# Optimization experiments

Hardware: AMD Instinct MI355X
Metric: run time of the kernel (lower is better)

## Reference

```python
import jax, jax.numpy as jnp
import numpy as np

NUM_HEADS = 8
EMBED_DIM = 64
HEAD_DIM = EMBED_DIM // NUM_HEADS
B, N, T = 2, 512, 24


def setup_inputs() -> dict:
    key = jax.random.key(0)
    ks = jax.random.split(key, 8)
    shp = (B, N, T, EMBED_DIM)
    return {
        "values": jax.random.normal(ks[0], shp, jnp.float32),
        "keys": jax.random.normal(ks[1], shp, jnp.float32),
        "query": jax.random.normal(ks[2], shp, jnp.float32),
        "Wv": jax.random.normal(ks[3], (HEAD_DIM, HEAD_DIM), jnp.float32) / np.sqrt(HEAD_DIM),
        "Wk": jax.random.normal(ks[4], (HEAD_DIM, HEAD_DIM), jnp.float32) / np.sqrt(HEAD_DIM),
        "Wq": jax.random.normal(ks[5], (HEAD_DIM, HEAD_DIM), jnp.float32) / np.sqrt(HEAD_DIM),
        "Wo": jax.random.normal(ks[6], (EMBED_DIM, EMBED_DIM), jnp.float32) / np.sqrt(EMBED_DIM),
        "bo": jnp.zeros((EMBED_DIM,), jnp.float32),
    }


def reference(values, keys, query, Wv, Wk, Wq, Wo, bo):
    b, n, t, e = query.shape
    h, d = NUM_HEADS, HEAD_DIM
    # split heads: (b, n, t, h, d)
    v = values.reshape(b, n, t, h, d) @ Wv.T
    k = keys.reshape(b, n, t, h, d) @ Wk.T
    q = query.reshape(b, n, t, h, d) @ Wq.T
    # node-axis attention per (timestep, head)
    energy = jnp.einsum('bqthd,bkthd->bqkth', q, k)  # (b, q_nodes, k_nodes, t, h)
    attn = jax.nn.softmax(energy / jnp.sqrt(jnp.float32(e)), axis=2)
    out = jnp.einsum('bqkth,bkthd->bqthd', attn, v).reshape(b, n, t, h * d)
    return out @ Wo.T + bo
```

## Files before the change

kernel.cpp:

```cpp
#include <hip/hip_runtime.h>

#define NUM_HEADS 8
#define EMBED 64
#define BB 2
#define NN 512
#define TT 24

typedef _Float16 half4v __attribute__((ext_vector_type(4)));
typedef _Float16 half2v __attribute__((ext_vector_type(2)));
typedef __fp16   fp16x2 __attribute__((ext_vector_type(2)));
typedef __fp16   fp16x4 __attribute__((ext_vector_type(4)));
typedef float    f32x4  __attribute__((ext_vector_type(4)));

#define KSTRIDE 20
#define VSTRIDE 524

__global__ __launch_bounds__(256) void attn_kernel(
    const float* __restrict__ values,
    const float* __restrict__ keys,
    const float* __restrict__ query,
    const float* __restrict__ Wv,
    const float* __restrict__ Wk,
    const float* __restrict__ Wq,
    float* __restrict__ out)
{
    __shared__ float w[192];
    __shared__ __align__(16) _Float16 Kpad[NN * KSTRIDE];
    __shared__ __align__(16) _Float16 Qpad[256 * KSTRIDE];
    __shared__ __align__(16) _Float16 Vt[16 * VSTRIDE];

    const int tid  = threadIdx.x;
    const int half = blockIdx.x >= 384;
    const int grp  = blockIdx.x - half * 384;
    const int h = grp & 7;
    const int t = (grp >> 3) % TT;
    const int b = grp / (8 * TT);

    const int r0 = 2 * tid;
    const long base0 = ((long)(b * NN + r0) * TT + t) * EMBED + h * 8;
    const long base1 = base0 + (long)TT * EMBED;
    const long qbase = ((long)(b * NN + half * 256 + tid) * TT + t) * EMBED + h * 8;
    float4 ka0 = *(const float4*)(keys + base0);
    float4 ka1 = *(const float4*)(keys + base0 + 4);
    float4 kb0 = *(const float4*)(keys + base1);
    float4 kb1 = *(const float4*)(keys + base1 + 4);
    float4 va0 = *(const float4*)(values + base0);
    float4 va1 = *(const float4*)(values + base0 + 4);
    float4 vb0 = *(const float4*)(values + base1);
    float4 vb1 = *(const float4*)(values + base1 + 4);
    float4 q0 = *(const float4*)(query + qbase);
    float4 q1 = *(const float4*)(query + qbase + 4);

    if (tid < 192) {
        float v;
        if (tid < 64)       v = Wq[tid];
        else if (tid < 128) v = Wk[tid - 64];
        else                v = Wv[tid - 128];
        w[tid] = v;
    }
    {
        unsigned int* z = (unsigned int*)(Vt + 8 * VSTRIDE);
        for (int i = tid; i < 8 * VSTRIDE / 2; i += 256)
            z[i] = (i < VSTRIDE / 2) ? 0x3C003C00u : 0u;
    }
    __syncthreads();

    {
        float k0[8] = {ka0.x, ka0.y, ka0.z, ka0.w, ka1.x, ka1.y, ka1.z, ka1.w};
        float k1[8] = {kb0.x, kb0.y, kb0.z, kb0.w, kb1.x, kb1.y, kb1.z, kb1.w};
        float v0[8] = {va0.x, va0.y, va0.z, va0.w, va1.x, va1.y, va1.z, va1.w};
        float v1[8] = {vb0.x, vb0.y, vb0.z, vb0.w, vb1.x, vb1.y, vb1.z, vb1.w};
        half4v klo0, khi0, klo1, khi1;
        #pragma unroll
        for (int dp = 0; dp < 8; ++dp) {
            float sk0 = 0.f, sk1 = 0.f, sv0 = 0.f, sv1 = 0.f;
            #pragma unroll
            for (int d = 0; d < 8; ++d) {
                const float wk = w[64 + dp * 8 + d], wvv = w[128 + dp * 8 + d];
                sk0 += k0[d] * wk;  sk1 += k1[d] * wk;
                sv0 += v0[d] * wvv; sv1 += v1[d] * wvv;
            }
            if (dp < 4) { klo0[dp] = (_Float16)sk0; klo1[dp] = (_Float16)sk1; }
            else        { khi0[dp - 4] = (_Float16)sk0; khi1[dp - 4] = (_Float16)sk1; }
            half2v vv = {(_Float16)sv0, (_Float16)sv1};
            *(half2v*)(Vt + dp * VSTRIDE + r0) = vv;
        }
        const half4v zz = {(_Float16)0.f, (_Float16)0.f, (_Float16)0.f, (_Float16)0.f};
        *(half4v*)(Kpad + r0 * KSTRIDE)            = klo0;
        *(half4v*)(Kpad + r0 * KSTRIDE + 4)        = khi0;
        *(half4v*)(Kpad + r0 * KSTRIDE + 8)        = zz;
        *(half4v*)(Kpad + r0 * KSTRIDE + 12)       = zz;
        *(half4v*)(Kpad + (r0 + 1) * KSTRIDE)      = klo1;
        *(half4v*)(Kpad + (r0 + 1) * KSTRIDE + 4)  = khi1;
        *(half4v*)(Kpad + (r0 + 1) * KSTRIDE + 8)  = zz;
        *(half4v*)(Kpad + (r0 + 1) * KSTRIDE + 12) = zz;

        float qx[8] = {q0.x, q0.y, q0.z, q0.w, q1.x, q1.y, q1.z, q1.w};
        const float scale = 0.125f * 1.44269504088896340736f;
        half4v qlo, qhi;
        #pragma unroll
        for (int dp = 0; dp < 8; ++dp) {
            float s = 0.f;
            #pragma unroll
            for (int d = 0; d < 8; ++d) s += qx[d] * w[dp * 8 + d];
            s *= scale;
            if (dp < 4) qlo[dp] = (_Float16)s; else qhi[dp - 4] = (_Float16)s;
        }
        *(half4v*)(Qpad + tid * KSTRIDE)      = qlo;
        *(half4v*)(Qpad + tid * KSTRIDE + 4)  = qhi;
        *(half4v*)(Qpad + tid * KSTRIDE + 8)  = zz;
        *(half4v*)(Qpad + tid * KSTRIDE + 12) = zz;
    }
    __syncthreads();

    const int wv   = tid >> 6;
    const int lane = tid & 63;
    const int ln   = lane & 15;
    const int quad = lane >> 4;
    const f32x4 zero4 = {0.f, 0.f, 0.f, 0.f};

    #pragma unroll 1
    for (int pass = 0; pass < 2; ++pass) {
        const int ql0 = pass * 128 + wv * 32;
        const half4v Qa = *(const half4v*)(Qpad + (ql0 + ln) * KSTRIDE + quad * 4);
        const half4v Qb = *(const half4v*)(Qpad + (ql0 + 16 + ln) * KSTRIDE + quad * 4);
        f32x4 Oa = {0.f, 0.f, 0.f, 0.f};
        f32x4 Ob = {0.f, 0.f, 0.f, 0.f};
        #pragma unroll 4
        for (int kt = 0; kt < 32; ++kt) {
            half4v Kf = *(const half4v*)(Kpad + (kt * 16 + ln) * KSTRIDE + quad * 4);
            half4v Vf = *(const half4v*)(Vt + ln * VSTRIDE + kt * 16 + quad * 4);
            f32x4 Ea = __builtin_amdgcn_mfma_f32_16x16x16f16(Kf, Qa, zero4, 0, 0, 0);
            f32x4 Eb = __builtin_amdgcn_mfma_f32_16x16x16f16(Kf, Qb, zero4, 0, 0, 0);
            fp16x2 pa0 = __builtin_amdgcn_cvt_pkrtz(__builtin_amdgcn_exp2f(Ea[0]),
                                                    __builtin_amdgcn_exp2f(Ea[1]));
            fp16x2 pa1 = __builtin_amdgcn_cvt_pkrtz(__builtin_amdgcn_exp2f(Ea[2]),
                                                    __builtin_amdgcn_exp2f(Ea[3]));
            fp16x2 pb0 = __builtin_amdgcn_cvt_pkrtz(__builtin_amdgcn_exp2f(Eb[0]),
                                                    __builtin_amdgcn_exp2f(Eb[1]));
            fp16x2 pb1 = __builtin_amdgcn_cvt_pkrtz(__builtin_amdgcn_exp2f(Eb[2]),
                                                    __builtin_amdgcn_exp2f(Eb[3]));
            half4v Pa = __builtin_bit_cast(half4v,
                (fp16x4)__builtin_shufflevector(pa0, pa1, 0, 1, 2, 3));
            half4v Pb = __builtin_bit_cast(half4v,
                (fp16x4)__builtin_shufflevector(pb0, pb1, 0, 1, 2, 3));
            Oa = __builtin_amdgcn_mfma_f32_16x16x16f16(Vf, Pa, Oa, 0, 0, 0);
            Ob = __builtin_amdgcn_mfma_f32_16x16x16f16(Vf, Pb, Ob, 0, 0, 0);
        }
        const float la = __shfl(Oa[0], 32 + ln, 64);
        const float lb = __shfl(Ob[0], 32 + ln, 64);
        const float ia = 1.0f / la;
        const float ib = 1.0f / lb;
        if (lane < 32) {
            const long oa = ((long)(b * NN + half * 256 + ql0 + ln) * TT + t) * EMBED
                          + h * 8 + quad * 4;
            const long ob = ((long)(b * NN + half * 256 + ql0 + 16 + ln) * TT + t) * EMBED
                          + h * 8 + quad * 4;
            *(float4*)(out + oa) = make_float4(Oa[0] * ia, Oa[1] * ia, Oa[2] * ia, Oa[3] * ia);
            *(float4*)(out + ob) = make_float4(Ob[0] * ib, Ob[1] * ib, Ob[2] * ib, Ob[3] * ib);
        }
    }
}

#define PSTRIDE 68
__global__ __launch_bounds__(256) void proj_kernel(
    const float* __restrict__ Wo,
    const float* __restrict__ bo,
    float* __restrict__ io)
{
    __shared__ float As[64 * PSTRIDE];
    __shared__ float WsT[64 * PSTRIDE];
    __shared__ float bos[EMBED];

    const int tid = threadIdx.x;
    const int row0 = blockIdx.x * 64;

    {
        const int r = tid >> 2;
        const int seg = tid & 3;
        #pragma unroll
        for (int i = 0; i < 4; ++i) {
            const int c = seg * 16 + i * 4;
            float4 av = *(const float4*)(io + (long)(row0 + r) * 64 + c);
            *(float4*)(As + r * PSTRIDE + c) = av;
        }
        #pragma unroll
        for (int i = 0; i < 16; ++i) {
            const int idx = tid + i * 256;
            WsT[(idx & 63) * PSTRIDE + (idx >> 6)] = Wo[idx];
        }
        if (tid < 64) bos[tid] = bo[tid];
    }
    __syncthreads();

    const int rg = tid >> 4;
    const int cg = tid & 15;
    float c[4][4] = {};
    #pragma unroll
    for (int kq = 0; kq < 16; ++kq) {
        float4 a[4], wt[4];
        #pragma unroll
        for (int i = 0; i < 4; ++i)
            a[i] = *(const float4*)(As + (rg * 4 + i) * PSTRIDE + kq * 4);
        #pragma unroll
        for (int kk = 0; kk < 4; ++kk)
            wt[kk] = *(const float4*)(WsT + (kq * 4 + kk) * PSTRIDE + cg * 4);
        #pragma unroll
        for (int i = 0; i < 4; ++i) {
            c[i][0] += a[i].x * wt[0].x + a[i].y * wt[1].x + a[i].z * wt[2].x + a[i].w * wt[3].x;
            c[i][1] += a[i].x * wt[0].y + a[i].y * wt[1].y + a[i].z * wt[2].y + a[i].w * wt[3].y;
            c[i][2] += a[i].x * wt[0].z + a[i].y * wt[1].z + a[i].z * wt[2].z + a[i].w * wt[3].z;
            c[i][3] += a[i].x * wt[0].w + a[i].y * wt[1].w + a[i].z * wt[2].w + a[i].w * wt[3].w;
        }
    }
    #pragma unroll
    for (int i = 0; i < 4; ++i) {
        float4 o = make_float4(c[i][0] + bos[cg * 4 + 0],
                               c[i][1] + bos[cg * 4 + 1],
                               c[i][2] + bos[cg * 4 + 2],
                               c[i][3] + bos[cg * 4 + 3]);
        *(float4*)(io + (long)(row0 + rg * 4 + i) * 64 + cg * 4) = o;
    }
}

extern "C" void kernel_launch(void* const* d_in, const int* in_sizes, int n_in,
                              void* d_out, int out_size, void* d_ws, size_t ws_size,
                              hipStream_t stream) {
    const float* values = (const float*)d_in[0];
    const float* keys   = (const float*)d_in[1];
    const float* query  = (const float*)d_in[2];
    const float* Wv     = (const float*)d_in[3];
    const float* Wk     = (const float*)d_in[4];
    const float* Wq     = (const float*)d_in[5];
    const float* Wo     = (const float*)d_in[6];
    const float* bo     = (const float*)d_in[7];
    float* out = (float*)d_out;

    (void)in_sizes; (void)n_in; (void)out_size; (void)d_ws; (void)ws_size;

    attn_kernel<<<BB * TT * NUM_HEADS * 2, 256, 0, stream>>>(
        values, keys, query, Wv, Wk, Wq, out);
    proj_kernel<<<(BB * NN * TT) / 64, 256, 0, stream>>>(Wo, bo, out);
}
```

Measured before the change: 116.4 us.

## Use fp16 MFMA for output projection and remap attention block indices

The output projection kernel is rewritten to drop its shared-memory fp32 FMA tiling. Each wavefront now loads 16 rows straight from global memory, converts them and Wo to fp16, and computes the result with 16x16x32 MFMA instructions, removing the LDS staging and the barrier. The attention kernel's block-to-(b,t,h,half) mapping is permuted so blocks are spread across XCDs differently, which may improve L2 locality for shared K/V data. The fp16 conversion lowers projection precision, and the output writes become scalar and strided.

```diff
diff --git a/kernel.cpp b/kernel.cpp
--- a/kernel.cpp
+++ b/kernel.cpp
@@ -8,6 +8,7 @@
 
 typedef _Float16 half4v __attribute__((ext_vector_type(4)));
 typedef _Float16 half2v __attribute__((ext_vector_type(2)));
+typedef _Float16 half8v __attribute__((ext_vector_type(8)));
 typedef __fp16   fp16x2 __attribute__((ext_vector_type(2)));
 typedef __fp16   fp16x4 __attribute__((ext_vector_type(4)));
 typedef float    f32x4  __attribute__((ext_vector_type(4)));
@@ -29,12 +30,15 @@
     __shared__ __align__(16) _Float16 Qpad[256 * KSTRIDE];
     __shared__ __align__(16) _Float16 Vt[16 * VSTRIDE];
 
-    const int tid  = threadIdx.x;
-    const int half = blockIdx.x >= 384;
-    const int grp  = blockIdx.x - half * 384;
-    const int h = grp & 7;
-    const int t = (grp >> 3) % TT;
-    const int b = grp / (8 * TT);
+    const int tid = threadIdx.x;
+    const int Bidx = blockIdx.x;
+    const int wi   = ((Bidx & 7) * 96) + (Bidx >> 3);
+    const int sub  = wi & 3;
+    const int rest = wi >> 2;
+    const int half = sub >> 1;
+    const int h    = ((rest & 3) << 1) | (sub & 1);
+    const int t    = (rest >> 2) % TT;
+    const int b    = rest / 96;
 
     const int r0 = 2 * tid;
     const long base0 = ((long)(b * NN + r0) * TT + t) * EMBED + h * 8;
@@ -162,64 +166,50 @@
     }
 }
 
-#define PSTRIDE 68
 __global__ __launch_bounds__(256) void proj_kernel(
     const float* __restrict__ Wo,
     const float* __restrict__ bo,
     float* __restrict__ io)
 {
-    __shared__ float As[64 * PSTRIDE];
-    __shared__ float WsT[64 * PSTRIDE];
-    __shared__ float bos[EMBED];
-
-    const int tid = threadIdx.x;
-    const int row0 = blockIdx.x * 64;
-
-    {
-        const int r = tid >> 2;
-        const int seg = tid & 3;
+    const int tid  = threadIdx.x;
+    const int wv   = tid >> 6;
+    const int lane = tid & 63;
+    const int ln   = lane & 15;
+    const int quad = lane >> 4;
+    const int row0 = blockIdx.x * 64 + wv * 16;
+
+    const float* arow = io + (long)(row0 + ln) * EMBED + quad * 8;
+    float4 a0 = *(const float4*)(arow);
+    float4 a1 = *(const float4*)(arow + 4);
+    float4 a2 = *(const float4*)(arow + 32);
+    float4 a3 = *(const float4*)(arow + 36);
+    half8v Af1, Af2;
+    Af1[0]=(_Float16)a0.x; Af1[1]=(_Float16)a0.y; Af1[2]=(_Float16)a0.z; Af1[3]=(_Float16)a0.w;
+    Af1[4]=(_Float16)a1.x; Af1[5]=(_Float16)a1.y; Af1[6]=(_Float16)a1.z; Af1[7]=(_Float16)a1.w;
+    Af2[0]=(_Float16)a2.x; Af2[1]=(_Float16)a2.y; Af2[2]=(_Float16)a2.z; Af2[3]=(_Float16)a2.w;
+    Af2[4]=(_Float16)a3.x; Af2[5]=(_Float16)a3.y; Af2[6]=(_Float16)a3.z; Af2[7]=(_Float16)a3.w;
+
+    #pragma unroll
+    for (int nt = 0; nt < 4; ++nt) {
+        const float* wrow = Wo + (long)(nt * 16 + ln) * EMBED + quad * 8;
+        float4 w0 = *(const float4*)(wrow);
+        float4 w1 = *(const float4*)(wrow + 4);
+        float4 w2 = *(const float4*)(wrow + 32);
+        float4 w3 = *(const float4*)(wrow + 36);
+        half8v Bf1, Bf2;
+        Bf1[0]=(_Float16)w0.x; Bf1[1]=(_Float16)w0.y; Bf1[2]=(_Float16)w0.z; Bf1[3]=(_Float16)w0.w;
+        Bf1[4]=(_Float16)w1.x; Bf1[5]=(_Float16)w1.y; Bf1[6]=(_Float16)w1.z; Bf1[7]=(_Float16)w1.w;
+        Bf2[0]=(_Float16)w2.x; Bf2[1]=(_Float16)w2.y; Bf2[2]=(_Float16)w2.z; Bf2[3]=(_Float16)w2.w;
+        Bf2[4]=(_Float16)w3.x; Bf2[5]=(_Float16)w3.y; Bf2[6]=(_Float16)w3.z; Bf2[7]=(_Float16)w3.w;
+
+        f32x4 D = {0.f, 0.f, 0.f, 0.f};
+        D = __builtin_amdgcn_mfma_f32_16x16x32_f16(Af1, Bf1, D, 0, 0, 0);
+        D = __builtin_amdgcn_mfma_f32_16x16x32_f16(Af2, Bf2, D, 0, 0, 0);
+
+        const float bias = bo[nt * 16 + ln];
         #pragma unroll
-        for (int i = 0; i < 4; ++i) {
-            const int c = seg * 16 + i * 4;
-            float4 av = *(const float4*)(io + (long)(row0 + r) * 64 + c);
-            *(float4*)(As + r * PSTRIDE + c) = av;
-        }
-        #pragma unroll
-        for (int i = 0; i < 16; ++i) {
-            const int idx = tid + i * 256;
-            WsT[(idx & 63) * PSTRIDE + (idx >> 6)] = Wo[idx];
-        }
-        if (tid < 64) bos[tid] = bo[tid];
-    }
-    __syncthreads();
-
-    const int rg = tid >> 4;
-    const int cg = tid & 15;
-    float c[4][4] = {};
-    #pragma unroll
-    for (int kq = 0; kq < 16; ++kq) {
-        float4 a[4], wt[4];
-        #pragma unroll
-        for (int i = 0; i < 4; ++i)
-            a[i] = *(const float4*)(As + (rg * 4 + i) * PSTRIDE + kq * 4);
-        #pragma unroll
-        for (int kk = 0; kk < 4; ++kk)
-            wt[kk] = *(const float4*)(WsT + (kq * 4 + kk) * PSTRIDE + cg * 4);
-        #pragma unroll
-        for (int i = 0; i < 4; ++i) {
-            c[i][0] += a[i].x * wt[0].x + a[i].y * wt[1].x + a[i].z * wt[2].x + a[i].w * wt[3].x;
-            c[i][1] += a[i].x * wt[0].y + a[i].y * wt[1].y + a[i].z * wt[2].y + a[i].w * wt[3].y;
-            c[i][2] += a[i].x * wt[0].z + a[i].y * wt[1].z + a[i].z * wt[2].z + a[i].w * wt[3].z;
-            c[i][3] += a[i].x * wt[0].w + a[i].y * wt[1].w + a[i].z * wt[2].w + a[i].w * wt[3].w;
-        }
-    }
-    #pragma unroll
-    for (int i = 0; i < 4; ++i) {
-        float4 o = make_float4(c[i][0] + bos[cg * 4 + 0],
-                               c[i][1] + bos[cg * 4 + 1],
-                               c[i][2] + bos[cg * 4 + 2],
-                               c[i][3] + bos[cg * 4 + 3]);
-        *(float4*)(io + (long)(row0 + rg * 4 + i) * 64 + cg * 4) = o;
+        for (int r = 0; r < 4; ++r)
+            io[(long)(row0 + quad * 4 + r) * EMBED + nt * 16 + ln] = D[r] + bias;
     }
 }
 
```

Result: faster. 105.2 us (-9.6%).
